# Performance work log

Hardware: AMD Instinct MI355X
Metric: run time of the kernel (lower is better)

## Reference

```python
import jax, jax.numpy as jnp
import numpy as np

T, N = 64, 128          # temporal / spatial graph sizes; M = T*N product-graph nodes
B, F_IN, HID, F_OUT = 2, 32, 32, 16
L, K = 2, 4             # num_layers, filter order


def _sym_norm(key, n):
    # random symmetric adjacency, then D^{-1/2} A D^{-1/2} / 2 as in the torch __init__
    a = jax.random.uniform(key, (n, n), dtype=jnp.float32)
    a = 0.5 * (a + a.T)
    d = jnp.sum(a, axis=1)
    dinv = 1.0 / jnp.sqrt(d)
    return (dinv[:, None] * a * dinv[None, :]) * 0.5


def setup_inputs() -> dict:
    key = jax.random.key(0)
    ks = jax.random.split(key, 9)
    x = jax.random.normal(ks[0], (B, T * N, F_IN), dtype=jnp.float32)
    Adj_t = _sym_norm(ks[1], T)
    Adj_s = _sym_norm(ks[2], N)
    s = jax.random.normal(ks[3], (4,), dtype=jnp.float32) * 0.25
    H = jax.random.normal(ks[4], (L, K, HID, HID), dtype=jnp.float32) * 0.1
    W1 = jax.random.normal(ks[5], (F_IN, HID), dtype=jnp.float32) * (1.0 / np.sqrt(F_IN))
    b1 = jax.random.normal(ks[6], (HID,), dtype=jnp.float32) * 0.01
    W2 = jax.random.normal(ks[7], (HID, F_OUT), dtype=jnp.float32) * (1.0 / np.sqrt(HID))
    b2 = jax.random.normal(ks[8], (F_OUT,), dtype=jnp.float32) * 0.01
    return {"x": x, "Adj_t": Adj_t, "Adj_s": Adj_s, "s": s, "H": H,
            "W1": W1, "b1": b1, "W2": W2, "b2": b2}


def reference(x, Adj_t, Adj_s, s, H, W1, b1, W2, b2):
    t, n = Adj_t.shape[0], Adj_s.shape[0]
    I_t = jnp.eye(t, dtype=jnp.float32)
    I_s = jnp.eye(n, dtype=jnp.float32)
    # Adj = s0*I + s1*kron(I_t, Adj_s) + s2*kron(Adj_t, I_s) + s3*kron(Adj_t, Adj_s)
    Adj = (s[0] * jnp.eye(t * n, dtype=jnp.float32)
           + s[1] * jnp.kron(I_t, Adj_s)
           + s[2] * jnp.kron(Adj_t, I_s)
           + s[3] * jnp.kron(Adj_t, Adj_s))
    h = x @ W1 + b1                                   # [B, M, HID]
    num_layers = H.shape[0]
    for l in range(num_layers):
        Ah = jnp.einsum('mn,bnh->bmh', Adj, h)        # Adj @ x, hoisted out of k-loop
        # sum_k (Adj@x) @ H[l,k]  ==  einsum over k and h simultaneously
        h = jnp.tanh(jnp.einsum('bmh,khf->bmf', Ah, H[l]))
    return h @ W2 + b2                                # [B, M, F_OUT]
```

## Files before the change

kernel.cpp:

```cpp
#include <hip/hip_runtime.h>

#define T_DIM 64
#define N_DIM 128
#define BATCH 2
#define F_IN  32
#define HIDW  32
#define F_OUT 16
#define KORD  4


template<bool PROJ>
__global__ __launch_bounds__(512) void k_temporal(
    const float* __restrict__ src,
    const float* __restrict__ At,
    const float* __restrict__ W1, const float* __restrict__ b1,
    const float* __restrict__ s,
    float* __restrict__ up, float* __restrict__ pp)
{
    __shared__ float At_s[64 * 65];
    __shared__ float h_loc[64 * 36];
    __shared__ float xs[64 * 33];
    __shared__ float W1s[32 * 32];

    const int tid = threadIdx.x;
    const int b   = blockIdx.x >> 7;
    const int n   = blockIdx.x & 127;
    const int fg  = tid >> 6;
    const int t   = tid & 63;

    const float s0v = s[0], s1v = s[1], s2v = s[2], s3v = s[3];

#pragma unroll
    for (int i = 0; i < 8; ++i) {
        int p = tid + 512 * i;
        At_s[(p >> 6) * 65 + (p & 63)] = At[p];
    }
    if (PROJ) {
        {
            int tt = tid >> 3, c4 = tid & 7;
            float4 v = *(const float4*)(src + ((size_t)(b * 8192 + tt * 128 + n)) * 32 + c4 * 4);
            float* dst = &xs[tt * 33 + c4 * 4];
            dst[0] = v.x; dst[1] = v.y; dst[2] = v.z; dst[3] = v.w;
        }
        if (tid < 256) ((float4*)W1s)[tid] = ((const float4*)W1)[tid];
    } else {
        int tt = tid >> 3, c4 = tid & 7;
        float4 v = *(const float4*)(src + ((size_t)(b * 128 + n)) * 2048 + tt * 32 + c4 * 4);
        *(float4*)&h_loc[tt * 36 + c4 * 4] = v;
    }
    __syncthreads();

    float h0, h1, h2, h3;
    if (PROJ) {
        float4 bv = *(const float4*)(b1 + fg * 4);
        h0 = bv.x; h1 = bv.y; h2 = bv.z; h3 = bv.w;
#pragma unroll 8
        for (int k = 0; k < 32; ++k) {
            float xv = xs[t * 33 + k];
            float4 wv = *(const float4*)(W1s + k * 32 + fg * 4);
            h0 += xv * wv.x; h1 += xv * wv.y; h2 += xv * wv.z; h3 += xv * wv.w;
        }
        float4 hv; hv.x = h0; hv.y = h1; hv.z = h2; hv.w = h3;
        *(float4*)&h_loc[t * 36 + fg * 4] = hv;
        __syncthreads();
    } else {
        float4 hv = *(const float4*)&h_loc[t * 36 + fg * 4];
        h0 = hv.x; h1 = hv.y; h2 = hv.z; h3 = hv.w;
    }

    float w0 = 0.f, w1 = 0.f, w2 = 0.f, w3 = 0.f;
#pragma unroll 4
    for (int u = 0; u < 64; ++u) {
        float a = At_s[t * 65 + u];
        float4 hv = *(const float4*)&h_loc[u * 36 + fg * 4];
        w0 += a * hv.x; w1 += a * hv.y; w2 += a * hv.z; w3 += a * hv.w;
    }
    float4 u4, p4;
    u4.x = s1v * h0 + s3v * w0;  p4.x = s0v * h0 + s2v * w0;
    u4.y = s1v * h1 + s3v * w1;  p4.y = s0v * h1 + s2v * w1;
    u4.z = s1v * h2 + s3v * w2;  p4.z = s0v * h2 + s2v * w2;
    u4.w = s1v * h3 + s3v * w3;  p4.w = s0v * h3 + s2v * w3;
    size_t base = ((size_t)((b * 64 + t) * 128 + n)) * 32 + fg * 4;
    *(float4*)(up + base) = u4;
    *(float4*)(pp + base) = p4;
}

template<bool LAST>
__global__ __launch_bounds__(512) void k_spatial(
    const float* __restrict__ up, const float* __restrict__ pp,
    const float* __restrict__ As, const float* __restrict__ H, int layer,
    const float* __restrict__ W2, const float* __restrict__ b2,
    float* __restrict__ hout, float* __restrict__ out)
{
    __shared__ float As_s[64 * 128];
    __shared__ float up_s[128 * 32];
    __shared__ float Ah_s[64 * 33];
    __shared__ float T_s[64 * 33];
    __shared__ float Hs[32 * 32];
    __shared__ float W2s[32 * 16];

    const int tid = threadIdx.x;
    const int b   = blockIdx.x >> 7;
    const int t   = (blockIdx.x >> 1) & 63;
    const int mh  = blockIdx.x & 1;
    const int fg  = tid >> 6;
    const int m   = tid & 63;

#pragma unroll
    for (int i = 0; i < 4; ++i) {
        int p = tid + 512 * i;
        int r = p >> 5, g = p & 31;
        float4 v = *(const float4*)(As + ((size_t)(mh * 64 + r)) * 128 + g * 4);
        *(float4*)&As_s[r * 128 + ((g ^ (r & 31)) << 2)] = v;
    }
    {
        const float4* srcu = (const float4*)(up + ((size_t)(b * 64 + t)) * 4096);
        float4* du = (float4*)up_s;
        du[tid]       = srcu[tid];
        du[tid + 512] = srcu[tid + 512];
    }
    {
        const float* Hl = H + layer * 4096;
        for (int i = tid; i < 1024; i += 512)
            Hs[i] = Hl[i] + Hl[1024 + i] + Hl[2048 + i] + Hl[3072 + i];
    }
    if (LAST) {
        if (tid < 128) ((float4*)W2s)[tid] = ((const float4*)W2)[tid];
    }
    float4 pv = *(const float4*)(pp + (((size_t)(b * 64 + t)) * 128 + mh * 64 + m) * 32 + fg * 4);
    float a0 = pv.x, a1 = pv.y, a2 = pv.z, a3 = pv.w;
    __syncthreads();

#pragma unroll 4
    for (int cu = 0; cu < 32; ++cu) {
        float4 av = *(const float4*)&As_s[m * 128 + ((cu ^ (m & 31)) << 2)];
        float4 u0 = *(const float4*)&up_s[(cu * 4 + 0) * 32 + fg * 4];
        float4 u1 = *(const float4*)&up_s[(cu * 4 + 1) * 32 + fg * 4];
        float4 u2 = *(const float4*)&up_s[(cu * 4 + 2) * 32 + fg * 4];
        float4 u3 = *(const float4*)&up_s[(cu * 4 + 3) * 32 + fg * 4];
        a0 += av.x * u0.x + av.y * u1.x + av.z * u2.x + av.w * u3.x;
        a1 += av.x * u0.y + av.y * u1.y + av.z * u2.y + av.w * u3.y;
        a2 += av.x * u0.z + av.y * u1.z + av.z * u2.z + av.w * u3.z;
        a3 += av.x * u0.w + av.y * u1.w + av.z * u2.w + av.w * u3.w;
    }
    Ah_s[m * 33 + fg * 4 + 0] = a0;
    Ah_s[m * 33 + fg * 4 + 1] = a1;
    Ah_s[m * 33 + fg * 4 + 2] = a2;
    Ah_s[m * 33 + fg * 4 + 3] = a3;
    __syncthreads();

    float c0 = 0.f, c1 = 0.f, c2 = 0.f, c3 = 0.f;
#pragma unroll 8
    for (int k = 0; k < 32; ++k) {
        float av = Ah_s[m * 33 + k];
        float4 hv = *(const float4*)&Hs[k * 32 + fg * 4];
        c0 += av * hv.x; c1 += av * hv.y; c2 += av * hv.z; c3 += av * hv.w;
    }
    c0 = tanhf(c0); c1 = tanhf(c1); c2 = tanhf(c2); c3 = tanhf(c3);

    if (!LAST) {
        float4 o; o.x = c0; o.y = c1; o.z = c2; o.w = c3;
        *(float4*)(hout + (((size_t)(b * 128 + mh * 64 + m)) * 64 + t) * 32 + fg * 4) = o;
    } else {
        T_s[m * 33 + fg * 4 + 0] = c0;
        T_s[m * 33 + fg * 4 + 1] = c1;
        T_s[m * 33 + fg * 4 + 2] = c2;
        T_s[m * 33 + fg * 4 + 3] = c3;
        __syncthreads();
        float o0 = b2[fg * 2], o1 = b2[fg * 2 + 1];
#pragma unroll 8
        for (int k = 0; k < 32; ++k) {
            float tv = T_s[m * 33 + k];
            o0 += tv * W2s[k * 16 + fg * 2];
            o1 += tv * W2s[k * 16 + fg * 2 + 1];
        }
        float2 o; o.x = o0; o.y = o1;
        *(float2*)(out + (((size_t)(b * 64 + t)) * 128 + mh * 64 + m) * 16 + fg * 2) = o;
    }
}

extern "C" void kernel_launch(void* const* d_in, const int* in_sizes, int n_in,
                              void* d_out, int out_size, void* d_ws, size_t ws_size,
                              hipStream_t stream)
{
    const float* x   = (const float*)d_in[0];
    const float* At  = (const float*)d_in[1];
    const float* As  = (const float*)d_in[2];
    const float* s   = (const float*)d_in[3];
    const float* H   = (const float*)d_in[4];
    const float* W1  = (const float*)d_in[5];
    const float* b1  = (const float*)d_in[6];
    const float* W2  = (const float*)d_in[7];
    const float* b2  = (const float*)d_in[8];
    float* out = (float*)d_out;

    const size_t SZ = (size_t)BATCH * T_DIM * N_DIM * HIDW;
    float* up = (float*)d_ws;
    float* pp = up + SZ;
    float* h  = pp + SZ;

    k_temporal<true ><<<BATCH * N_DIM, 512, 0, stream>>>(x, At, W1, b1, s, up, pp);
    k_spatial <false><<<BATCH * T_DIM * 2, 512, 0, stream>>>(up, pp, As, H, 0, W2, b2, h, out);
    k_temporal<false><<<BATCH * N_DIM, 512, 0, stream>>>(h, At, W1, b1, s, up, pp);
    k_spatial <true ><<<BATCH * T_DIM * 2, 512, 0, stream>>>(up, pp, As, H, 1, W2, b2, h, out);
}
```

Measured before the change: 33.14 us.

## Read wave-uniform operands directly from global memory and precompute summed H once

```diff
diff --git a/kernel.cpp b/kernel.cpp
--- a/kernel.cpp
+++ b/kernel.cpp
@@ -3,11 +3,10 @@
 #define T_DIM 64
 #define N_DIM 128
 #define BATCH 2
-#define F_IN  32
 #define HIDW  32
-#define F_OUT 16
-#define KORD  4
-
+
+
+__device__ __forceinline__ int rfl(int x) { return __builtin_amdgcn_readfirstlane(x); }
 
 template<bool PROJ>
 __global__ __launch_bounds__(512) void k_temporal(
@@ -15,89 +14,110 @@
     const float* __restrict__ At,
     const float* __restrict__ W1, const float* __restrict__ b1,
     const float* __restrict__ s,
+    const float* __restrict__ H, float* __restrict__ Hsum_ws,
     float* __restrict__ up, float* __restrict__ pp)
 {
-    __shared__ float At_s[64 * 65];
+    __shared__ float At_s[64 * 68];
+    __shared__ float xs[64 * 36];
     __shared__ float h_loc[64 * 36];
-    __shared__ float xs[64 * 33];
-    __shared__ float W1s[32 * 32];
 
     const int tid = threadIdx.x;
     const int b   = blockIdx.x >> 7;
     const int n   = blockIdx.x & 127;
     const int fg  = tid >> 6;
     const int t   = tid & 63;
+    const int fg4u = rfl(fg * 4);
 
     const float s0v = s[0], s1v = s[1], s2v = s[2], s3v = s[3];
+
+    if (PROJ && blockIdx.x < 4) {
+        int idx = blockIdx.x * 512 + tid;
+        int l = idx >> 10, rem = idx & 1023;
+        const float* Hl = H + l * 4096;
+        Hsum_ws[idx] = Hl[rem] + Hl[1024 + rem] + Hl[2048 + rem] + Hl[3072 + rem];
+    }
 
 #pragma unroll
     for (int i = 0; i < 8; ++i) {
         int p = tid + 512 * i;
-        At_s[(p >> 6) * 65 + (p & 63)] = At[p];
-    }
+        At_s[(p >> 6) * 68 + (p & 63)] = At[p];
+    }
+
+    float h0, h1, h2, h3;
     if (PROJ) {
         {
             int tt = tid >> 3, c4 = tid & 7;
             float4 v = *(const float4*)(src + ((size_t)(b * 8192 + tt * 128 + n)) * 32 + c4 * 4);
-            float* dst = &xs[tt * 33 + c4 * 4];
-            dst[0] = v.x; dst[1] = v.y; dst[2] = v.z; dst[3] = v.w;
-        }
-        if (tid < 256) ((float4*)W1s)[tid] = ((const float4*)W1)[tid];
-    } else {
-        int tt = tid >> 3, c4 = tid & 7;
-        float4 v = *(const float4*)(src + ((size_t)(b * 128 + n)) * 2048 + tt * 32 + c4 * 4);
-        *(float4*)&h_loc[tt * 36 + c4 * 4] = v;
-    }
-    __syncthreads();
-
-    float h0, h1, h2, h3;
-    if (PROJ) {
-        float4 bv = *(const float4*)(b1 + fg * 4);
+            *(float4*)&xs[tt * 36 + c4 * 4] = v;
+        }
+        __syncthreads();
+        const float* W1u = W1 + fg4u;
+        float4 bv = *(const float4*)(b1 + fg4u);
         h0 = bv.x; h1 = bv.y; h2 = bv.z; h3 = bv.w;
-#pragma unroll 8
-        for (int k = 0; k < 32; ++k) {
-            float xv = xs[t * 33 + k];
-            float4 wv = *(const float4*)(W1s + k * 32 + fg * 4);
-            h0 += xv * wv.x; h1 += xv * wv.y; h2 += xv * wv.z; h3 += xv * wv.w;
+#pragma unroll
+        for (int k4 = 0; k4 < 8; ++k4) {
+            float4 xv = *(const float4*)&xs[t * 36 + k4 * 4];
+            float4 w0 = *(const float4*)(W1u + (k4 * 4 + 0) * 32);
+            float4 w1 = *(const float4*)(W1u + (k4 * 4 + 1) * 32);
+            float4 w2 = *(const float4*)(W1u + (k4 * 4 + 2) * 32);
+            float4 w3 = *(const float4*)(W1u + (k4 * 4 + 3) * 32);
+            h0 += xv.x * w0.x + xv.y * w1.x + xv.z * w2.x + xv.w * w3.x;
+            h1 += xv.x * w0.y + xv.y * w1.y + xv.z * w2.y + xv.w * w3.y;
+            h2 += xv.x * w0.z + xv.y * w1.z + xv.z * w2.z + xv.w * w3.z;
+            h3 += xv.x * w0.w + xv.y * w1.w + xv.z * w2.w + xv.w * w3.w;
         }
         float4 hv; hv.x = h0; hv.y = h1; hv.z = h2; hv.w = h3;
         *(float4*)&h_loc[t * 36 + fg * 4] = hv;
         __syncthreads();
     } else {
-        float4 hv = *(const float4*)&h_loc[t * 36 + fg * 4];
+        __syncthreads();
+        float4 hv = *(const float4*)(src + (((size_t)(b * 128 + n)) * 64 + t) * 32 + fg * 4);
         h0 = hv.x; h1 = hv.y; h2 = hv.z; h3 = hv.w;
     }
 
     float w0 = 0.f, w1 = 0.f, w2 = 0.f, w3 = 0.f;
-#pragma unroll 4
-    for (int u = 0; u < 64; ++u) {
-        float a = At_s[t * 65 + u];
-        float4 hv = *(const float4*)&h_loc[u * 36 + fg * 4];
-        w0 += a * hv.x; w1 += a * hv.y; w2 += a * hv.z; w3 += a * hv.w;
-    }
-    float4 u4, p4;
-    u4.x = s1v * h0 + s3v * w0;  p4.x = s0v * h0 + s2v * w0;
-    u4.y = s1v * h1 + s3v * w1;  p4.y = s0v * h1 + s2v * w1;
-    u4.z = s1v * h2 + s3v * w2;  p4.z = s0v * h2 + s2v * w2;
-    u4.w = s1v * h3 + s3v * w3;  p4.w = s0v * h3 + s2v * w3;
+    const float* hrow = PROJ ? nullptr
+                             : (src + rfl((b * 128 + n) * 2048) + fg4u);
+#pragma unroll
+    for (int u4 = 0; u4 < 16; ++u4) {
+        float4 av = *(const float4*)&At_s[t * 68 + u4 * 4];
+        float4 g0, g1, g2, g3;
+        if (PROJ) {
+            g0 = *(const float4*)&h_loc[(u4 * 4 + 0) * 36 + fg * 4];
+            g1 = *(const float4*)&h_loc[(u4 * 4 + 1) * 36 + fg * 4];
+            g2 = *(const float4*)&h_loc[(u4 * 4 + 2) * 36 + fg * 4];
+            g3 = *(const float4*)&h_loc[(u4 * 4 + 3) * 36 + fg * 4];
+        } else {
+            g0 = *(const float4*)(hrow + (u4 * 4 + 0) * 32);
+            g1 = *(const float4*)(hrow + (u4 * 4 + 1) * 32);
+            g2 = *(const float4*)(hrow + (u4 * 4 + 2) * 32);
+            g3 = *(const float4*)(hrow + (u4 * 4 + 3) * 32);
+        }
+        w0 += av.x * g0.x + av.y * g1.x + av.z * g2.x + av.w * g3.x;
+        w1 += av.x * g0.y + av.y * g1.y + av.z * g2.y + av.w * g3.y;
+        w2 += av.x * g0.z + av.y * g1.z + av.z * g2.z + av.w * g3.z;
+        w3 += av.x * g0.w + av.y * g1.w + av.z * g2.w + av.w * g3.w;
+    }
+    float4 u4v, p4v;
+    u4v.x = s1v * h0 + s3v * w0;  p4v.x = s0v * h0 + s2v * w0;
+    u4v.y = s1v * h1 + s3v * w1;  p4v.y = s0v * h1 + s2v * w1;
+    u4v.z = s1v * h2 + s3v * w2;  p4v.z = s0v * h2 + s2v * w2;
+    u4v.w = s1v * h3 + s3v * w3;  p4v.w = s0v * h3 + s2v * w3;
     size_t base = ((size_t)((b * 64 + t) * 128 + n)) * 32 + fg * 4;
-    *(float4*)(up + base) = u4;
-    *(float4*)(pp + base) = p4;
+    *(float4*)(up + base) = u4v;
+    *(float4*)(pp + base) = p4v;
 }
 
 template<bool LAST>
 __global__ __launch_bounds__(512) void k_spatial(
     const float* __restrict__ up, const float* __restrict__ pp,
-    const float* __restrict__ As, const float* __restrict__ H, int layer,
+    const float* __restrict__ As, const float* __restrict__ Hsum_ws, int layer,
     const float* __restrict__ W2, const float* __restrict__ b2,
     float* __restrict__ hout, float* __restrict__ out)
 {
-    __shared__ float As_s[64 * 128];
-    __shared__ float up_s[128 * 32];
-    __shared__ float Ah_s[64 * 33];
-    __shared__ float T_s[64 * 33];
-    __shared__ float Hs[32 * 32];
-    __shared__ float W2s[32 * 16];
+    __shared__ float As_s[64 * 132];
+    __shared__ float Ah_s[64 * 36];
+    __shared__ float T_s[64 * 36];
 
     const int tid = threadIdx.x;
     const int b   = blockIdx.x >> 7;
@@ -105,56 +125,51 @@
     const int mh  = blockIdx.x & 1;
     const int fg  = tid >> 6;
     const int m   = tid & 63;
+    const int fg4u = rfl(fg * 4);
 
 #pragma unroll
     for (int i = 0; i < 4; ++i) {
         int p = tid + 512 * i;
         int r = p >> 5, g = p & 31;
         float4 v = *(const float4*)(As + ((size_t)(mh * 64 + r)) * 128 + g * 4);
-        *(float4*)&As_s[r * 128 + ((g ^ (r & 31)) << 2)] = v;
-    }
-    {
-        const float4* srcu = (const float4*)(up + ((size_t)(b * 64 + t)) * 4096);
-        float4* du = (float4*)up_s;
-        du[tid]       = srcu[tid];
-        du[tid + 512] = srcu[tid + 512];
-    }
-    {
-        const float* Hl = H + layer * 4096;
-        for (int i = tid; i < 1024; i += 512)
-            Hs[i] = Hl[i] + Hl[1024 + i] + Hl[2048 + i] + Hl[3072 + i];
-    }
-    if (LAST) {
-        if (tid < 128) ((float4*)W2s)[tid] = ((const float4*)W2)[tid];
+        *(float4*)&As_s[r * 132 + g * 4] = v;
     }
     float4 pv = *(const float4*)(pp + (((size_t)(b * 64 + t)) * 128 + mh * 64 + m) * 32 + fg * 4);
     float a0 = pv.x, a1 = pv.y, a2 = pv.z, a3 = pv.w;
     __syncthreads();
 
-#pragma unroll 4
-    for (int cu = 0; cu < 32; ++cu) {
-        float4 av = *(const float4*)&As_s[m * 128 + ((cu ^ (m & 31)) << 2)];
-        float4 u0 = *(const float4*)&up_s[(cu * 4 + 0) * 32 + fg * 4];
-        float4 u1 = *(const float4*)&up_s[(cu * 4 + 1) * 32 + fg * 4];
-        float4 u2 = *(const float4*)&up_s[(cu * 4 + 2) * 32 + fg * 4];
-        float4 u3 = *(const float4*)&up_s[(cu * 4 + 3) * 32 + fg * 4];
+    const float* urow = up + rfl((b * 64 + t) * 4096) + fg4u;
+#pragma unroll 8
+    for (int n4 = 0; n4 < 32; ++n4) {
+        float4 av = *(const float4*)&As_s[m * 132 + n4 * 4];
+        float4 u0 = *(const float4*)(urow + (n4 * 4 + 0) * 32);
+        float4 u1 = *(const float4*)(urow + (n4 * 4 + 1) * 32);
+        float4 u2 = *(const float4*)(urow + (n4 * 4 + 2) * 32);
+        float4 u3 = *(const float4*)(urow + (n4 * 4 + 3) * 32);
         a0 += av.x * u0.x + av.y * u1.x + av.z * u2.x + av.w * u3.x;
         a1 += av.x * u0.y + av.y * u1.y + av.z * u2.y + av.w * u3.y;
         a2 += av.x * u0.z + av.y * u1.z + av.z * u2.z + av.w * u3.z;
         a3 += av.x * u0.w + av.y * u1.w + av.z * u2.w + av.w * u3.w;
     }
-    Ah_s[m * 33 + fg * 4 + 0] = a0;
-    Ah_s[m * 33 + fg * 4 + 1] = a1;
-    Ah_s[m * 33 + fg * 4 + 2] = a2;
-    Ah_s[m * 33 + fg * 4 + 3] = a3;
+    {
+        float4 w; w.x = a0; w.y = a1; w.z = a2; w.w = a3;
+        *(float4*)&Ah_s[m * 36 + fg * 4] = w;
+    }
     __syncthreads();
 
+    const float* hsrow = Hsum_ws + rfl(layer * 1024) + fg4u;
     float c0 = 0.f, c1 = 0.f, c2 = 0.f, c3 = 0.f;
-#pragma unroll 8
-    for (int k = 0; k < 32; ++k) {
-        float av = Ah_s[m * 33 + k];
-        float4 hv = *(const float4*)&Hs[k * 32 + fg * 4];
-        c0 += av * hv.x; c1 += av * hv.y; c2 += av * hv.z; c3 += av * hv.w;
+#pragma unroll
+    for (int k4 = 0; k4 < 8; ++k4) {
+        float4 av = *(const float4*)&Ah_s[m * 36 + k4 * 4];
+        float4 q0 = *(const float4*)(hsrow + (k4 * 4 + 0) * 32);
+        float4 q1 = *(const float4*)(hsrow + (k4 * 4 + 1) * 32);
+        float4 q2 = *(const float4*)(hsrow + (k4 * 4 + 2) * 32);
+        float4 q3 = *(const float4*)(hsrow + (k4 * 4 + 3) * 32);
+        c0 += av.x * q0.x + av.y * q1.x + av.z * q2.x + av.w * q3.x;
+        c1 += av.x * q0.y + av.y * q1.y + av.z * q2.y + av.w * q3.y;
+        c2 += av.x * q0.z + av.y * q1.z + av.z * q2.z + av.w * q3.z;
+        c3 += av.x * q0.w + av.y * q1.w + av.z * q2.w + av.w * q3.w;
     }
     c0 = tanhf(c0); c1 = tanhf(c1); c2 = tanhf(c2); c3 = tanhf(c3);
 
@@ -162,17 +177,21 @@
         float4 o; o.x = c0; o.y = c1; o.z = c2; o.w = c3;
         *(float4*)(hout + (((size_t)(b * 128 + mh * 64 + m)) * 64 + t) * 32 + fg * 4) = o;
     } else {
-        T_s[m * 33 + fg * 4 + 0] = c0;
-        T_s[m * 33 + fg * 4 + 1] = c1;
-        T_s[m * 33 + fg * 4 + 2] = c2;
-        T_s[m * 33 + fg * 4 + 3] = c3;
-        __syncthreads();
-        float o0 = b2[fg * 2], o1 = b2[fg * 2 + 1];
-#pragma unroll 8
-        for (int k = 0; k < 32; ++k) {
-            float tv = T_s[m * 33 + k];
-            o0 += tv * W2s[k * 16 + fg * 2];
-            o1 += tv * W2s[k * 16 + fg * 2 + 1];
+        float4 w; w.x = c0; w.y = c1; w.z = c2; w.w = c3;
+        *(float4*)&T_s[m * 36 + fg * 4] = w;
+        __syncthreads();
+        const int fg2u = rfl(fg * 2);
+        float o0 = b2[fg2u], o1 = b2[fg2u + 1];
+        const float* w2r = W2 + fg2u;
+#pragma unroll
+        for (int k4 = 0; k4 < 8; ++k4) {
+            float4 tv = *(const float4*)&T_s[m * 36 + k4 * 4];
+            float2 v0 = *(const float2*)(w2r + (k4 * 4 + 0) * 16);
+            float2 v1 = *(const float2*)(w2r + (k4 * 4 + 1) * 16);
+            float2 v2 = *(const float2*)(w2r + (k4 * 4 + 2) * 16);
+            float2 v3 = *(const float2*)(w2r + (k4 * 4 + 3) * 16);
+            o0 += tv.x * v0.x + tv.y * v1.x + tv.z * v2.x + tv.w * v3.x;
+            o1 += tv.x * v0.y + tv.y * v1.y + tv.z * v2.y + tv.w * v3.y;
         }
         float2 o; o.x = o0; o.y = o1;
         *(float2*)(out + (((size_t)(b * 64 + t)) * 128 + mh * 64 + m) * 16 + fg * 2) = o;
@@ -194,13 +213,13 @@
     const float* b2  = (const float*)d_in[8];
     float* out = (float*)d_out;
 
-    const size_t SZ = (size_t)BATCH * T_DIM * N_DIM * HIDW;
-    float* up = (float*)d_ws;
-    float* pp = up + SZ;
-    float* h  = pp + SZ;
-
-    k_temporal<true ><<<BATCH * N_DIM, 512, 0, stream>>>(x, At, W1, b1, s, up, pp);
-    k_spatial <false><<<BATCH * T_DIM * 2, 512, 0, stream>>>(up, pp, As, H, 0, W2, b2, h, out);
-    k_temporal<false><<<BATCH * N_DIM, 512, 0, stream>>>(h, At, W1, b1, s, up, pp);
-    k_spatial <true ><<<BATCH * T_DIM * 2, 512, 0, stream>>>(up, pp, As, H, 1, W2, b2, h, out);
+    float* up   = (float*)d_ws;
+    float* pp   = up + 524288;
+    float* h    = pp + 524288;
+    float* Hsum = h  + 524288;
+
+    k_temporal<true ><<<256, 512, 0, stream>>>(x, At, W1, b1, s, H, Hsum, up, pp);
+    k_spatial <false><<<256, 512, 0, stream>>>(up, pp, As, Hsum, 0, W2, b2, h, out);
+    k_temporal<false><<<256, 512, 0, stream>>>(h, At, W1, b1, s, H, Hsum, up, pp);
+    k_spatial <true ><<<256, 512, 0, stream>>>(up, pp, As, Hsum, 1, W2, b2, h, out);
 }
```

After: 40.13 us. 1.21x slower.
